# Kernel optimization log

Hardware: AMD Instinct MI355X
Metric: run time of the kernel (lower is better)

## Reference

```python
import jax, jax.numpy as jnp
import numpy as np

HID = 2048      # hidden_size
NH = 32         # num_heads
QLR = 1536      # q_lora_rank
KVLR = 512      # kv_lora_rank
DR = 64         # qk_rope_head_dim
DN = 128        # qk_nope_head_dim
DV = 128        # v_head_dim
DQK = DN + DR   # 192
EPS = 1e-6
ROPE_BASE = 10000.0


def rms_norm(x, w):
    return x * jax.lax.rsqrt(jnp.mean(x * x, axis=-1, keepdims=True) + EPS) * w


def apply_rope(x, pos):
    # x: [B, S, H, d] (non-interleaved / rotate-half convention), pos: [S]
    d = x.shape[-1]
    inv_freq = 1.0 / (ROPE_BASE ** (jnp.arange(0, d, 2, dtype=jnp.float32) / d))
    freqs = pos[:, None].astype(jnp.float32) * inv_freq      # [S, d/2]
    cos = jnp.cos(freqs)[None, :, None, :]                   # [1, S, 1, d/2]
    sin = jnp.sin(freqs)[None, :, None, :]
    x1, x2 = x[..., : d // 2], x[..., d // 2:]
    return jnp.concatenate([x1 * cos - x2 * sin, x1 * sin + x2 * cos], axis=-1)


def setup_inputs() -> dict:
    key = jax.random.key(0)
    ks = jax.random.split(key, 8)
    s = 0.02
    return {
        "hidden_states": jax.random.normal(ks[0], (1, 2048, HID), jnp.float32),
        "q_a_w":    jax.random.normal(ks[1], (HID, QLR), jnp.float32) * s,
        "q_a_ln_w": jnp.ones((QLR,), jnp.float32),
        "q_b_w":    jax.random.normal(ks[2], (QLR, NH * DQK), jnp.float32) * s,
        "kv_a_w":   jax.random.normal(ks[3], (HID, KVLR + DR), jnp.float32) * s,
        "kv_a_ln_w": jnp.ones((KVLR,), jnp.float32),
        "kv_b_w":   jax.random.normal(ks[4], (KVLR, NH * (DN + DV)), jnp.float32) * s,
        "o_w":      jax.random.normal(ks[5], (NH * DV, HID), jnp.float32) * s,
    }


def reference(hidden_states, q_a_w, q_a_ln_w, q_b_w, kv_a_w, kv_a_ln_w, kv_b_w, o_w):
    B, S, _ = hidden_states.shape
    # low-rank Q: down-proj -> RMSNorm -> up-proj
    q = rms_norm(hidden_states @ q_a_w, q_a_ln_w) @ q_b_w       # [B,S,NH*DQK]
    q = q.reshape(B, S, NH, DQK)
    q_pass, q_rot = q[..., :DN], q[..., DN:]
    # compressed KV + shared rope key
    ckv = hidden_states @ kv_a_w                                # [B,S,KVLR+DR]
    c_kv, k_rot = ckv[..., :KVLR], ckv[..., KVLR:]
    kv = rms_norm(c_kv, kv_a_ln_w) @ kv_b_w                     # [B,S,NH*(DN+DV)]
    kv = kv.reshape(B, S, NH, DN + DV)
    k_pass, v = kv[..., :DN], kv[..., DN:]
    # RoPE
    pos = jnp.arange(S)
    q_rot = apply_rope(q_rot, pos)                              # [B,S,NH,DR]
    k_rot = apply_rope(k_rot[:, :, None, :], pos)[:, :, 0, :]   # [B,S,DR] (shared head)
    # causal attention, scale = qk_head_dim**-0.5
    scale = DQK ** -0.5
    scores = (jnp.einsum('bqhd,bkhd->bhqk', q_pass, k_pass)
              + jnp.einsum('bqhd,bkd->bhqk', q_rot, k_rot)) * scale
    causal = jnp.tril(jnp.ones((S, S), dtype=bool))
    scores = jnp.where(causal[None, None], scores, jnp.finfo(scores.dtype).min)
    p = jax.nn.softmax(scores, axis=-1)
    out = jnp.einsum('bhqk,bkhd->bqhd', p, v).reshape(B, S, NH * DV)
    return out @ o_w
```

## Files before the change

### kernel.cpp

```cpp
#include <hip/hip_runtime.h>


typedef __bf16 bf16x8 __attribute__((ext_vector_type(8)));
typedef float  f32x4  __attribute__((ext_vector_type(4)));
typedef unsigned u32x4 __attribute__((ext_vector_type(4)));

#define GLOAD16(g, l)                                                          \
  __builtin_amdgcn_global_load_lds(                                            \
      (const __attribute__((address_space(1))) unsigned int*)(g),              \
      (__attribute__((address_space(3))) unsigned int*)(l), 16, 0, 0)

__device__ __forceinline__ unsigned short f2b(float f) {
  unsigned u = __builtin_bit_cast(unsigned, f);
  u += 0x7fffu + ((u >> 16) & 1u);
  return (unsigned short)(u >> 16);
}

__device__ __forceinline__ unsigned cvtpk(float lo, float hi) {
  unsigned r;
  asm("v_cvt_pk_bf16_f32 %0, %1, %2" : "=v"(r) : "v"(lo), "v"(hi));
  return r;
}

__device__ __forceinline__ void tc_body(const float* __restrict__ src,
// ... 31 lines not shown
    return;
  }
  b -= 4096;
  int tx = tid & 31, ty = tid >> 5;
  if (b < 3072)       { tc_body(qaw,  wcat,               2048, 1536, b & 63,  b >> 6, tx, ty); return; }
  b -= 3072;
  if (b < 1280)       { tc_body(kvaw, wcat + 1536UL*2048, 2048, 576,  b & 63,  b >> 6, tx, ty); return; }
  b -= 1280;
  if (b < 9216)       { tc_body(qbw,  qbT,                1536, 6144, b % 48,  b / 48, tx, ty); return; }
  b -= 9216;
  if (b < 4096)       { tc_body(kvbw, kvbT,               512,  8192, b & 15,  b >> 4, tx, ty); return; }
  b -= 4096;
  tc_body(ow, owT, 4096, 2048, b & 127, b >> 7, tx, ty);
}

__global__ __launch_bounds__(256) void rms2(const float* __restrict__ c0,
                                            const float* __restrict__ c1,
                                            const float* __restrict__ qw,
                                            const float* __restrict__ kvw,
                                            unsigned short* __restrict__ qan,
                                            unsigned short* __restrict__ ckvn,
                                            unsigned short* __restrict__ Kb) {
  int b = blockIdx.x, tid = threadIdx.x;
  __shared__ float red[4];
  if (b < 2048) {
    const float* x0 = c0 + (size_t)b * 2176;
    const float* x1 = c1 + (size_t)b * 2176;
    float vb[6], ss = 0.f;
#pragma unroll
    for (int j = 0; j < 6; j++) {
      float v = x0[tid + j * 256] + x1[tid + j * 256];
      vb[j] = v; ss += v * v;
    }
#pragma unroll
    for (int off = 1; off < 64; off <<= 1) ss += __shfl_xor(ss, off, 64);
    if ((tid & 63) == 0) red[tid >> 6] = ss;
    __syncthreads();
    ss = red[0] + red[1] + red[2] + red[3];
    float r = rsqrtf(ss / 1536.f + 1e-6f);
    unsigned short* orow = qan + (size_t)b * 1536;
#pragma unroll
    for (int j = 0; j < 6; j++)
      orow[tid + j * 256] = f2b(vb[j] * r * qw[tid + j * 256]);
  } else {
    int t = b - 2048;
    const float* x0 = c0 + (size_t)t * 2176 + 1536;
    const float* x1 = c1 + (size_t)t * 2176 + 1536;
    float vb[2], ss = 0.f;
#pragma unroll
    for (int j = 0; j < 2; j++) {
      float v = x0[tid + j * 256] + x1[tid + j * 256];
      vb[j] = v; ss += v * v;
    }
#pragma unroll
    for (int off = 1; off < 64; off <<= 1) ss += __shfl_xor(ss, off, 64);
    __shared__ unsigned short rot[64];
    if ((tid & 63) == 0) red[tid >> 6] = ss;
    __syncthreads();
    ss = red[0] + red[1] + red[2] + red[3];
    float r = rsqrtf(ss / 512.f + 1e-6f);
    unsigned short* orow = ckvn + (size_t)t * 512;
#pragma unroll
    for (int j = 0; j < 2; j++)
      orow[tid + j * 256] = f2b(vb[j] * r * kvw[tid + j * 256]);
    if (tid < 32) {
      float x1v = c0[(size_t)t * 2176 + 2048 + tid] + c1[(size_t)t * 2176 + 2048 + tid];
      float x2v = c0[(size_t)t * 2176 + 2080 + tid] + c1[(size_t)t * 2176 + 2080 + tid];
      float a = (float)t * exp2f(-(float)tid * 0.4152410118609203f);
      float cs = __cosf(a), sn = __sinf(a);
      rot[tid]      = f2b(x1v * cs - x2v * sn);
      rot[tid + 32] = f2b(x1v * sn + x2v * cs);
    }
    __syncthreads();
    for (int idx = tid; idx < 2048; idx += 256) {
      int h = idx >> 6, d = idx & 63;
      Kb[(size_t)t * 6144 + h * 192 + 128 + d] = rot[d];
    }
  }
}

__global__ __launch_bounds__(256) void addout(const float4* __restrict__ p,
                                              float4* __restrict__ o) {
  int i = blockIdx.x * 256 + threadIdx.x;
  float4 a = p[i], b = p[i + 1048576];
  float4 r; r.x = a.x + b.x; r.y = a.y + b.y; r.z = a.z + b.z; r.w = a.w + b.w;
  o[i] = r;
}

__global__ __launch_bounds__(256) void gemm_bt(const unsigned short* __restrict__ A,
                                               const unsigned short* __restrict__ Bt,
                                               float* __restrict__ Cp,
                                               int M, int N, int Ktot,
                                               int GX, int total) {
  __shared__ unsigned short As[4096];
  __shared__ unsigned short Bs[4096];
  const int tid = threadIdx.x;
  const int w = tid >> 6, lane = tid & 63;
  const int lr = lane & 15, lh = lane >> 4;
  const int lin = blockIdx.x, cpx = gridDim.x >> 3;
  int sid = (lin & 7) * cpx + (lin >> 3);
  const int s = (sid >= total);
  if (s) sid -= total;
  const int m0 = (sid / GX) * 128, n0 = (sid % GX) * 128;
  const int Kseg = Ktot >> 1;
  const unsigned short* Ab = A + (size_t)s * Kseg;
  const unsigned short* Bb = Bt + (size_t)s * Kseg;
  float* C = Cp + (size_t)s * M * N;
  const int wm = w >> 1, wn = w & 1;
  const int srow = lane >> 2;
  const int schunk = (lane & 3) ^ ((lane >> 3) & 3);
  const int swzr = (lr >> 1) & 3;

  f32x4 acc[4][4];
  const f32x4 z = {0.f, 0.f, 0.f, 0.f};
#pragma unroll
  for (int i = 0; i < 4; i++)
#pragma unroll
    for (int j = 0; j < 4; j++) acc[i][j] = z;

  for (int k0 = 0; k0 < Kseg; k0 += 32) {
#pragma unroll
    for (int c = 0; c < 2; c++) {
      GLOAD16(Ab + (size_t)(m0 + c * 64 + w * 16 + srow) * Ktot + k0 + schunk * 8,
              As + c * 2048 + w * 512);
      GLOAD16(Bb + (size_t)(n0 + c * 64 + w * 16 + srow) * Ktot + k0 + schunk * 8,
              Bs + c * 2048 + w * 512);
    }
    __syncthreads();
    bf16x8 a[4], b[4];
#pragma unroll
    for (int m = 0; m < 4; m++) {
      int row = wm * 64 + m * 16 + lr;
      a[m] = *(const bf16x8*)(As + row * 32 + ((lh ^ swzr) * 8));
    }
#pragma unroll
    for (int n = 0; n < 4; n++) {
      int row = wn * 64 + n * 16 + lr;
      b[n] = *(const bf16x8*)(Bs + row * 32 + ((lh ^ swzr) * 8));
    }
#pragma unroll
    for (int m = 0; m < 4; m++)
#pragma unroll
      for (int n = 0; n < 4; n++)
        acc[m][n] = __builtin_amdgcn_mfma_f32_16x16x32_bf16(a[m], b[n], acc[m][n], 0, 0, 0);
    __syncthreads();
  }
#pragma unroll
  for (int m = 0; m < 4; m++)
#pragma unroll
    for (int n = 0; n < 4; n++)
#pragma unroll
      for (int r = 0; r < 4; r++) {
        int row = m0 + wm * 64 + m * 16 + lh * 4 + r;
        int col = n0 + wn * 64 + n * 16 + lr;
        C[(size_t)row * N + col] = acc[m][n][r];
      }
}

__global__ __launch_bounds__(512) void gemm256m(
    const unsigned short* __restrict__ Aq, const unsigned short* __restrict__ Bq,
    unsigned short* __restrict__ Qb,
    const unsigned short* __restrict__ Akv, const unsigned short* __restrict__ Bkv,
    unsigned short* __restrict__ Kb, unsigned short* __restrict__ Vt) {
  __shared__ unsigned short lds[2][2][16384];
  const int tid = threadIdx.x;
  const int w = tid >> 6, lane = tid & 63;
  const int lr = lane & 15, lh = lane >> 4;
  const int wr = w >> 2, wc = w & 3;
  const int blk = blockIdx.x;
  const bool isq = blk < 192;
  const int bx = isq ? (blk % 24) : ((blk - 192) & 31);
  const int by = isq ? (blk / 24) : ((blk - 192) >> 5);
  const int K  = isq ? 1536 : 512;
  const int N  = isq ? 6144 : 8192;
  const unsigned short* A  = isq ? Aq : Akv;
  const unsigned short* Bt = isq ? Bq : Bkv;
  const int m0 = by * 256, n0 = bx * 256;

  int soff[2];
#pragma unroll
  for (int j = 0; j < 2; j++) {
    int c = j * 512 + tid;
    int row = c >> 3, p = c & 7;
    soff[j] = row * K + (p ^ (row & 7)) * 8;
  }
  const unsigned short* Abase = A + (size_t)m0 * K;
  const unsigned short* Bbase = Bt + (size_t)n0 * K;
  const int rswz = lr & 7;

#define STAGEOP(op, Base, kt, buf)                                             \
  {                                                                            \
    _Pragma("unroll") for (int hh = 0; hh < 2; hh++)                           \
    _Pragma("unroll") for (int j = 0; j < 2; j++)                              \
      GLOAD16(Base + (size_t)(hh * 128) * K + soff[j] + (kt) * 64,             \
              &lds[buf][op][(hh * 1024 + j * 512 + w * 64) * 8]);              \
  }
#define READA(mh, buf)                                                         \
  {                                                                            \
    _Pragma("unroll") for (int mi = 0; mi < 4; mi++)                           \
    _Pragma("unroll") for (int ks = 0; ks < 2; ks++)                           \
      af[mi][ks] = *(const bf16x8*)&lds[buf][0][                               \
          (wr * 128 + ((mh) * 4 + mi) * 16 + lr) * 64 +                        \
          (((ks * 4 + lh) ^ rswz) * 8)];                                       \
  }
#define READB(n, buf)                                                          \
  {                                                                            \
    _Pragma("unroll") for (int ks = 0; ks < 2; ks++)                           \
      bfr[n][ks] = *(const bf16x8*)&lds[buf][1][                               \
          (wc * 64 + (n) * 16 + lr) * 64 + (((ks * 4 + lh) ^ rswz) * 8)];      \
  }
#define MFMAQ(mh, nh)                                                          \
  {                                                                            \
    __builtin_amdgcn_s_setprio(1);                                             \
    _Pragma("unroll") for (int mi = 0; mi < 4; mi++)                           \
    _Pragma("unroll") for (int ni = 0; ni < 2; ni++)                           \
    _Pragma("unroll") for (int ks = 0; ks < 2; ks++)                           \
      acc[(mh) * 4 + mi][(nh) * 2 + ni] =                                      \
          __builtin_amdgcn_mfma_f32_16x16x32_bf16(                             \
              af[mi][ks], bfr[(nh) * 2 + ni][ks],                              \
              acc[(mh) * 4 + mi][(nh) * 2 + ni], 0, 0, 0);                     \
    __builtin_amdgcn_s_setprio(0);                                             \
  }

  f32x4 acc[8][4];
  const f32x4 z = {0.f, 0.f, 0.f, 0.f};
#pragma unroll
  for (int i = 0; i < 8; i++)
#pragma unroll
    for (int j = 0; j < 4; j++) acc[i][j] = z;

  STAGEOP(0, Abase, 0, 0);
  STAGEOP(1, Bbase, 0, 0);
  asm volatile("s_waitcnt vmcnt(0)" ::: "memory");
  __builtin_amdgcn_s_barrier();

  const int KT = K >> 6;
  for (int kt = 0; kt < KT; ++kt) {
    const int buf = kt & 1;
    const bool more = (kt + 1 < KT);
    bf16x8 af[4][2], bfr[4][2];
    READA(0, buf);
    READB(0, buf); READB(1, buf);
    if (more) STAGEOP(0, Abase, kt + 1, buf ^ 1);
    __builtin_amdgcn_s_barrier();
    MFMAQ(0, 0);
    __builtin_amdgcn_s_barrier();
    READB(2, buf); READB(3, buf);
    if (more) STAGEOP(1, Bbase, kt + 1, buf ^ 1);
    __builtin_amdgcn_s_barrier();
    MFMAQ(0, 1);
    __builtin_amdgcn_s_barrier();
    READA(1, buf);
    __builtin_amdgcn_s_barrier();
    MFMAQ(1, 1);
    __builtin_amdgcn_s_barrier();
    MFMAQ(1, 0);
    if (more) asm volatile("s_waitcnt vmcnt(0)" ::: "memory");
    __builtin_amdgcn_s_barrier();
  }
#undef STAGEOP
#undef READA
#undef READB
#undef MFMAQ

  if (isq) {
    const float kSc = 0.104126984f;
#pragma unroll
    for (int m = 0; m < 8; m++)
#pragma unroll
      for (int n = 0; n < 4; n++) {
        int colb = n0 + wc * 64 + n * 16;
        int sb = colb % 192;
        bool isrope = sb >= 128;
        bool first  = sb < 160;
        int col = colb + lr;
#pragma unroll
        for (int r = 0; r < 4; r++) {
          int row = m0 + wr * 128 + m * 16 + lh * 4 + r;
          float v = acc[m][n][r], o;
          if (!isrope) {
            o = v;
          } else {
            int ii = (col - 128) & 31;
            float ang = (float)row * exp2f(-(float)ii * 0.4152410118609203f);
            float cs = __cosf(ang), sn = __sinf(ang);
            float pa_ = acc[m][(n + 2) & 3][r];
            float pb_ = acc[m][(n + 6) & 3][r];
            float partner = first ? pa_ : pb_;
            o = first ? (v * cs - partner * sn) : (partner * sn + v * cs);
          }
          Qb[(size_t)row * 6144 + col] = f2b(o * kSc);
        }
      }
  } else {
    const int h = bx;
    unsigned short* Vlds = (unsigned short*)lds;
    if (wc < 2) {
#pragma unroll
      for (int m = 0; m < 8; m++)
#pragma unroll
        for (int n = 0; n < 4; n++) {
          int dd = wc * 64 + n * 16 + lr;
          int rowb = m0 + wr * 128 + m * 16 + lh * 4;
#pragma unroll
          for (int r = 0; r < 4; r++)
            Kb[(size_t)(rowb + r) * 6144 + h * 192 + dd] = f2b(acc[m][n][r]);
        }
    } else {
#pragma unroll
      for (int m = 0; m < 8; m++)
#pragma unroll
        for (int n = 0; n < 4; n++) {
          int dd = (wc - 2) * 64 + n * 16 + lr;
          int tl = wr * 128 + m * 16 + lh * 4;
          ushort4 pk;
          pk.x = f2b(acc[m][n][0]); pk.y = f2b(acc[m][n][1]);
          pk.z = f2b(acc[m][n][2]); pk.w = f2b(acc[m][n][3]);
          *(ushort4*)(Vlds + dd * 264 + tl) = pk;
        }
    }
    __syncthreads();
    {
      int r = tid >> 2, seg = tid & 3;
      const unsigned short* srcp = Vlds + r * 264 + seg * 64;
      unsigned short* dstp = Vt + (size_t)(h * 128 + r) * 2048 + m0 + seg * 64;
#pragma unroll
      for (int j = 0; j < 8; j++)
        *(int4*)(dstp + j * 8) = *(const int4*)(srcp + j * 8);
    }
  }
}

__global__ __launch_bounds__(512) void attn(const unsigned short* __restrict__ Qb,
                                            const unsigned short* __restrict__ Kb,
                                            const unsigned short* __restrict__ Vt,
                                            unsigned short* __restrict__ O) {
  __shared__ unsigned short Kl[2][12288];
  __shared__ unsigned short Vl[2][8192];
  const int tid = threadIdx.x;
  const int w = tid >> 6, lane = tid & 63;
  const int lr = lane & 15, lh = lane >> 4;
  const int b = blockIdx.x;
  const int x = b & 7, k = b >> 3;
  const int h = x + 8 * (k >> 4);
  const int ii = k & 15;
  int qi = (ii & 1) ? (15 - 2 * (ii >> 1)) : (2 * (ii >> 1));
  if (k & 32) qi = 15 - qi;
  const int q0 = qi * 128;
  const int qw = q0 + w * 16;
  const int qv = qw + lr;

  bf16x8 qf[6];
#pragma unroll
  for (int c = 0; c < 6; c++)
    qf[c] = *(const bf16x8*)(Qb + (size_t)(qw + lr) * 6144 + h * 192 + c * 32 + lh * 8);

  const unsigned short* Kbase = Kb + h * 192;
  const unsigned short* Vbase = Vt + (size_t)h * 128 * 2048;
  size_t ka[3];
#pragma unroll
  for (int j = 0; j < 3; j++) {
    int c = tid + j * 512;
    int r = c / 24, p = c - r * 24;
    ka[j] = (size_t)r * 6144 + (p ^ (r & 7)) * 8;
  }
  size_t va[2];
#pragma unroll
  for (int j = 0; j < 2; j++) {
    int c = tid + j * 512;
    int d = c >> 3, p = c & 7;
    va[j] = (size_t)d * 2048 + (p ^ (d & 7)) * 8;
  }

#define STAGE(T0, B)                                                           \
  {                                                                            \
    _Pragma("unroll") for (int j = 0; j < 3; j++)                              \
        GLOAD16(Kbase + (size_t)(T0) * 6144 + ka[j], &Kl[B][(tid + j * 512) * 8]); \
    _Pragma("unroll") for (int j = 0; j < 2; j++)                              \
        GLOAD16(Vbase + va[j] + (T0), &Vl[B][(tid + j * 512) * 8]);            \
  }

  f32x4 acc[8];
  const f32x4 z = {0.f, 0.f, 0.f, 0.f};
#pragma unroll
  for (int n = 0; n < 8; n++) acc[n] = z;
  float mrow = -1e30f, lrow = 0.f;
  const int swz = (lr & 7) * 8;
  const int cv0 = ((lh ^ (lr & 7)) * 8);
  const int cv1 = (((4 + lh) ^ (lr & 7)) * 8);
  const int sA = lr + 32 * (lh & 1), sB = sA + 16;

  const int nt = (q0 + 128) >> 6;
  STAGE(0, 0);
  __syncthreads();
  for (int it = 0; it < nt; ++it) {
    const int t0 = it << 6;
    const int cur = it & 1;
    if (it + 1 < nt) STAGE(t0 + 64, cur ^ 1);
    if (t0 <= qw + 15) {
      f32x4 s0 = z, s1 = z, s2 = z, s3 = z;
      __builtin_amdgcn_s_setprio(1);
#pragma unroll
      for (int c = 0; c < 6; c++) {
        int col = ((c * 4 + lh) * 8) ^ swz;
        bf16x8 k0 = *(const bf16x8*)(&Kl[cur][(lr)      * 192 + col]);
        bf16x8 k1 = *(const bf16x8*)(&Kl[cur][(16 + lr) * 192 + col]);
        bf16x8 k2 = *(const bf16x8*)(&Kl[cur][(32 + lr) * 192 + col]);
        bf16x8 k3 = *(const bf16x8*)(&Kl[cur][(48 + lr) * 192 + col]);
        s0 = __builtin_amdgcn_mfma_f32_16x16x32_bf16(k0, qf[c], s0, 0, 0, 0);
        s1 = __builtin_amdgcn_mfma_f32_16x16x32_bf16(k1, qf[c], s1, 0, 0, 0);
        s2 = __builtin_amdgcn_mfma_f32_16x16x32_bf16(k2, qf[c], s2, 0, 0, 0);
        s3 = __builtin_amdgcn_mfma_f32_16x16x32_bf16(k3, qf[c], s3, 0, 0, 0);
      }
      __builtin_amdgcn_s_setprio(0);
      const int tb = t0 + lh * 4;
      if (t0 + 63 > qw) {
#pragma unroll
        for (int r = 0; r < 4; r++) {
          s0[r] = (tb + r > qv)      ? -1e30f : s0[r];
          s1[r] = (tb + 16 + r > qv) ? -1e30f : s1[r];
          s2[r] = (tb + 32 + r > qv) ? -1e30f : s2[r];
          s3[r] = (tb + 48 + r > qv) ? -1e30f : s3[r];
        }
      }
      float mx = -1e30f;
#pragma unroll
      for (int r = 0; r < 4; r++)
        mx = fmaxf(mx, fmaxf(fmaxf(s0[r], s1[r]), fmaxf(s2[r], s3[r])));
      mx = fmaxf(mx, __shfl_xor(mx, 16, 64));
      mx = fmaxf(mx, __shfl_xor(mx, 32, 64));
      float ro = 1.f;
      bool resc = (mx - mrow) > 11.5f;
      if (resc) { ro = exp2f(mrow - mx); mrow = mx; }
      float p0[4], p1[4], p2[4], p3[4], ls = 0.f;
#pragma unroll
      for (int r = 0; r < 4; r++) {
        p0[r] = exp2f(s0[r] - mrow);
        p1[r] = exp2f(s1[r] - mrow);
        p2[r] = exp2f(s2[r] - mrow);
        p3[r] = exp2f(s3[r] - mrow);
        ls += (p0[r] + p1[r]) + (p2[r] + p3[r]);
      }
      lrow = lrow * ro + ls;
      if (__any(resc)) {
        float rs[4];
#pragma unroll
        for (int r = 0; r < 4; r++) rs[r] = __shfl(ro, lh * 4 + r, 16);
#pragma unroll
        for (int n = 0; n < 8; n++)
#pragma unroll
          for (int r = 0; r < 4; r++) acc[n][r] *= rs[r];
      }
      unsigned k0p = cvtpk(p0[0], p0[1]), k1p = cvtpk(p0[2], p0[3]);
      unsigned k2p = cvtpk(p1[0], p1[1]), k3p = cvtpk(p1[2], p1[3]);
      unsigned k4p = cvtpk(p2[0], p2[1]), k5p = cvtpk(p2[2], p2[3]);
      unsigned k6p = cvtpk(p3[0], p3[1]), k7p = cvtpk(p3[2], p3[3]);
      u32x4 w0, w1;
      {
        unsigned A0 = __shfl(k0p, sA, 64), A1 = __shfl(k1p, sA, 64);
        unsigned B0 = __shfl(k0p, sB, 64), B1 = __shfl(k1p, sB, 64);
        unsigned C0 = __shfl(k2p, sA, 64), C1 = __shfl(k3p, sA, 64);
        unsigned D0 = __shfl(k2p, sB, 64), D1 = __shfl(k3p, sB, 64);
        w0[0] = (lh < 2) ? A0 : C0;
        w0[1] = (lh < 2) ? A1 : C1;
        w0[2] = (lh < 2) ? B0 : D0;
        w0[3] = (lh < 2) ? B1 : D1;
      }
      {
        unsigned A0 = __shfl(k4p, sA, 64), A1 = __shfl(k5p, sA, 64);
        unsigned B0 = __shfl(k4p, sB, 64), B1 = __shfl(k5p, sB, 64);
        unsigned C0 = __shfl(k6p, sA, 64), C1 = __shfl(k7p, sA, 64);
        unsigned D0 = __shfl(k6p, sB, 64), D1 = __shfl(k7p, sB, 64);
        w1[0] = (lh < 2) ? A0 : C0;
        w1[1] = (lh < 2) ? A1 : C1;
        w1[2] = (lh < 2) ? B0 : D0;
        w1[3] = (lh < 2) ? B1 : D1;
      }
      bf16x8 pa0 = __builtin_bit_cast(bf16x8, w0);
      bf16x8 pa1 = __builtin_bit_cast(bf16x8, w1);
      __builtin_amdgcn_s_setprio(1);
#pragma unroll
      for (int n = 0; n < 8; n++) {
        bf16x8 vb0 = *(const bf16x8*)(&Vl[cur][(n * 16 + lr) * 64 + cv0]);
        bf16x8 vb1 = *(const bf16x8*)(&Vl[cur][(n * 16 + lr) * 64 + cv1]);
        acc[n] = __builtin_amdgcn_mfma_f32_16x16x32_bf16(pa0, vb0, acc[n], 0, 0, 0);
        acc[n] = __builtin_amdgcn_mfma_f32_16x16x32_bf16(pa1, vb1, acc[n], 0, 0, 0);
      }
      __builtin_amdgcn_s_setprio(0);
    }
    __syncthreads();
  }
#undef STAGE
  lrow += __shfl_xor(lrow, 16, 64);
  lrow += __shfl_xor(lrow, 32, 64);
  float invL = 1.f / lrow;
  float inv[4];
#pragma unroll
  for (int r = 0; r < 4; r++) inv[r] = __shfl(invL, lh * 4 + r, 16);
#pragma unroll
  for (int n = 0; n < 8; n++)
#pragma unroll
    for (int r = 0; r < 4; r++) {
      int q = qw + lh * 4 + r;
      O[(size_t)q * 4096 + h * 128 + n * 16 + lr] = f2b(acc[n][r] * inv[r]);
    }
}

extern "C" void kernel_launch(void* const* d_in, const int* in_sizes, int n_in,
                              void* d_out, int out_size, void* d_ws, size_t ws_size,
                              hipStream_t stream) {
  const float* hs      = (const float*)d_in[0];
  const float* q_a_w   = (const float*)d_in[1];
  const float* q_a_ln  = (const float*)d_in[2];
  const float* q_b_w   = (const float*)d_in[3];
  const float* kv_a_w  = (const float*)d_in[4];
  const float* kv_a_ln = (const float*)d_in[5];
  const float* kv_b_w  = (const float*)d_in[6];
  const float* o_w     = (const float*)d_in[7];
  float* out = (float*)d_out;

  char* ws = (char*)d_ws;
  size_t off = 0;
  auto alloc = [&](size_t bytes) {
    void* p = ws + off;
    off += (bytes + 255) & ~(size_t)255;
    return p;
  };
  unsigned short* wcat    = (unsigned short*)alloc(2176UL * 2048 * 2);
  unsigned short* q_b_wT  = (unsigned short*)alloc(6144UL * 1536 * 2);
  unsigned short* kv_b_wT = (unsigned short*)alloc(8192UL * 512 * 2);
  unsigned short* o_wT    = (unsigned short*)alloc(2048UL * 4096 * 2);
  unsigned short* hs_b    = (unsigned short*)alloc(2048UL * 2048 * 2);
  unsigned short* q_a_n   = (unsigned short*)alloc(2048UL * 1536 * 2);
  unsigned short* Qb      = (unsigned short*)alloc(2048UL * 6144 * 2);
  unsigned short* ckv_n   = (unsigned short*)alloc(2048UL * 512 * 2);
  unsigned short* Kb      = (unsigned short*)alloc(2048UL * 6144 * 2);
  unsigned short* Vt      = (unsigned short*)alloc(32UL * 128 * 2048 * 2);
  char* big = (char*)alloc(37748736UL + 2UL * 2048 * 2048 * 4);
  float*          Craw0    = (float*)big;
  float*          Craw1    = (float*)(big + 2048UL * 2176 * 4);
  unsigned short* attn_out = (unsigned short*)big;
  float*          OutP     = (float*)(big + 37748736UL);
  (void)ws_size; (void)in_sizes; (void)n_in; (void)out_size;

  dim3 b256(256), b512(512);
  prep<<<29952, b256, 0, stream>>>(hs, hs_b, q_a_w, kv_a_w, wcat,
                                   q_b_w, q_b_wT, kv_b_w, kv_b_wT, o_w, o_wT);
  gemm_bt<<<544, b256, 0, stream>>>(hs_b, wcat, Craw0, 2048, 2176, 2048, 17, 272);
  rms2<<<4096, b256, 0, stream>>>(Craw0, Craw1, q_a_ln, kv_a_ln, q_a_n, ckv_n, Kb);
  gemm256m<<<448, b512, 0, stream>>>(q_a_n, q_b_wT, Qb, ckv_n, kv_b_wT, Kb, Vt);
  attn<<<512, b512, 0, stream>>>(Qb, Kb, Vt, attn_out);
  gemm_bt<<<512, b256, 0, stream>>>(attn_out, o_wT, OutP, 2048, 2048, 4096, 16, 256);
  addout<<<4096, b256, 0, stream>>>((const float4*)OutP, (float4*)out);
}
```

Baseline: 298.2 us.

## Halve attention KV tile to 32 keys and split o-proj GEMM four ways

The attention kernel now stages 32-key K/V tiles instead of 64, halving LDS use and cutting the work per iteration to two score MFMAs and one PV MFMA per output block. The V LDS swizzle is redone for the narrower tile. This gives finer causal skipping and a lower LDS footprint per block, at the cost of twice as many loop iterations and barriers. Separately, the output projection GEMM becomes a 4-way split-K over 1024 blocks for more parallelism, writing its partials into the reused Qb buffer, with addout summing four partials instead of two.

```diff
diff --git a/kernel.cpp b/kernel.cpp
--- a/kernel.cpp
+++ b/kernel.cpp
@@ -137,8 +137,12 @@
 __global__ __launch_bounds__(256) void addout(const float4* __restrict__ p,
                                               float4* __restrict__ o) {
   int i = blockIdx.x * 256 + threadIdx.x;
-  float4 a = p[i], b = p[i + 1048576];
-  float4 r; r.x = a.x + b.x; r.y = a.y + b.y; r.z = a.z + b.z; r.w = a.w + b.w;
+  float4 a = p[i], b = p[i + 1048576], c = p[i + 2097152], d = p[i + 3145728];
+  float4 r;
+  r.x = (a.x + b.x) + (c.x + d.x);
+  r.y = (a.y + b.y) + (c.y + d.y);
+  r.z = (a.z + b.z) + (c.z + d.z);
+  r.w = (a.w + b.w) + (c.w + d.w);
   o[i] = r;
 }
 
@@ -146,7 +150,7 @@
                                                const unsigned short* __restrict__ Bt,
                                                float* __restrict__ Cp,
                                                int M, int N, int Ktot,
-                                               int GX, int total) {
+                                               int GX, int total, int splits) {
   __shared__ unsigned short As[4096];
   __shared__ unsigned short Bs[4096];
   const int tid = threadIdx.x;
@@ -154,10 +158,10 @@
   const int lr = lane & 15, lh = lane >> 4;
   const int lin = blockIdx.x, cpx = gridDim.x >> 3;
   int sid = (lin & 7) * cpx + (lin >> 3);
-  const int s = (sid >= total);
-  if (s) sid -= total;
+  const int s = sid / total;
+  sid -= s * total;
   const int m0 = (sid / GX) * 128, n0 = (sid % GX) * 128;
-  const int Kseg = Ktot >> 1;
+  const int Kseg = Ktot / splits;
   const unsigned short* Ab = A + (size_t)s * Kseg;
   const unsigned short* Bb = Bt + (size_t)s * Kseg;
   float* C = Cp + (size_t)s * M * N;
@@ -390,8 +394,8 @@
                                             const unsigned short* __restrict__ Kb,
                                             const unsigned short* __restrict__ Vt,
                                             unsigned short* __restrict__ O) {
-  __shared__ unsigned short Kl[2][12288];
-  __shared__ unsigned short Vl[2][8192];
+  __shared__ unsigned short Kl[2][6144];
+  __shared__ unsigned short Vl[2][4096];
   const int tid = threadIdx.x;
   const int w = tid >> 6, lane = tid & 63;
   const int lr = lane & 15, lh = lane >> 4;
@@ -412,27 +416,30 @@
 
   const unsigned short* Kbase = Kb + h * 192;
   const unsigned short* Vbase = Vt + (size_t)h * 128 * 2048;
-  size_t ka[3];
-#pragma unroll
-  for (int j = 0; j < 3; j++) {
-    int c = tid + j * 512;
+  size_t kga0, kga1 = 0;
+  {
+    int c = w * 64 + lane;
     int r = c / 24, p = c - r * 24;
-    ka[j] = (size_t)r * 6144 + (p ^ (r & 7)) * 8;
-  }
-  size_t va[2];
-#pragma unroll
-  for (int j = 0; j < 2; j++) {
-    int c = tid + j * 512;
-    int d = c >> 3, p = c & 7;
-    va[j] = (size_t)d * 2048 + (p ^ (d & 7)) * 8;
+    kga0 = (size_t)r * 6144 + (p ^ (r & 7)) * 8;
+  }
+  if (w < 4) {
+    int c = 512 + w * 64 + lane;
+    int r = c / 24, p = c - r * 24;
+    kga1 = (size_t)r * 6144 + (p ^ (r & 7)) * 8;
+  }
+  size_t vga;
+  {
+    int c = w * 64 + lane;
+    int d = c >> 2, p = c & 3;
+    vga = (size_t)d * 2048 + (p ^ ((d >> 1) & 3)) * 8;
   }
 
 #define STAGE(T0, B)                                                           \
   {                                                                            \
-    _Pragma("unroll") for (int j = 0; j < 3; j++)                              \
-        GLOAD16(Kbase + (size_t)(T0) * 6144 + ka[j], &Kl[B][(tid + j * 512) * 8]); \
-    _Pragma("unroll") for (int j = 0; j < 2; j++)                              \
-        GLOAD16(Vbase + va[j] + (T0), &Vl[B][(tid + j * 512) * 8]);            \
+    GLOAD16(Kbase + (size_t)(T0) * 6144 + kga0, &Kl[B][w * 512]);              \
+    if (w < 4)                                                                 \
+      GLOAD16(Kbase + (size_t)(T0) * 6144 + kga1, &Kl[B][4096 + w * 512]);     \
+    GLOAD16(Vbase + vga + (T0), &Vl[B][w * 512]);                              \
   }
 
   f32x4 acc[8];
@@ -441,60 +448,51 @@
   for (int n = 0; n < 8; n++) acc[n] = z;
   float mrow = -1e30f, lrow = 0.f;
   const int swz = (lr & 7) * 8;
-  const int cv0 = ((lh ^ (lr & 7)) * 8);
-  const int cv1 = (((4 + lh) ^ (lr & 7)) * 8);
+  const int vsw = (lh ^ ((lr >> 1) & 3)) * 8;
   const int sA = lr + 32 * (lh & 1), sB = sA + 16;
 
-  const int nt = (q0 + 128) >> 6;
+  const int nt = (q0 + 128) >> 5;
   STAGE(0, 0);
   __syncthreads();
   for (int it = 0; it < nt; ++it) {
-    const int t0 = it << 6;
+    const int t0 = it << 5;
     const int cur = it & 1;
-    if (it + 1 < nt) STAGE(t0 + 64, cur ^ 1);
+    if (it + 1 < nt) STAGE(t0 + 32, cur ^ 1);
     if (t0 <= qw + 15) {
-      f32x4 s0 = z, s1 = z, s2 = z, s3 = z;
+      f32x4 s0 = z, s1 = z;
       __builtin_amdgcn_s_setprio(1);
 #pragma unroll
       for (int c = 0; c < 6; c++) {
         int col = ((c * 4 + lh) * 8) ^ swz;
-        bf16x8 k0 = *(const bf16x8*)(&Kl[cur][(lr)      * 192 + col]);
+        bf16x8 k0 = *(const bf16x8*)(&Kl[cur][lr * 192 + col]);
         bf16x8 k1 = *(const bf16x8*)(&Kl[cur][(16 + lr) * 192 + col]);
-        bf16x8 k2 = *(const bf16x8*)(&Kl[cur][(32 + lr) * 192 + col]);
-        bf16x8 k3 = *(const bf16x8*)(&Kl[cur][(48 + lr) * 192 + col]);
         s0 = __builtin_amdgcn_mfma_f32_16x16x32_bf16(k0, qf[c], s0, 0, 0, 0);
         s1 = __builtin_amdgcn_mfma_f32_16x16x32_bf16(k1, qf[c], s1, 0, 0, 0);
-        s2 = __builtin_amdgcn_mfma_f32_16x16x32_bf16(k2, qf[c], s2, 0, 0, 0);
-        s3 = __builtin_amdgcn_mfma_f32_16x16x32_bf16(k3, qf[c], s3, 0, 0, 0);
       }
       __builtin_amdgcn_s_setprio(0);
       const int tb = t0 + lh * 4;
-      if (t0 + 63 > qw) {
+      if (t0 + 31 > qw) {
 #pragma unroll
         for (int r = 0; r < 4; r++) {
           s0[r] = (tb + r > qv)      ? -1e30f : s0[r];
           s1[r] = (tb + 16 + r > qv) ? -1e30f : s1[r];
-          s2[r] = (tb + 32 + r > qv) ? -1e30f : s2[r];
-          s3[r] = (tb + 48 + r > qv) ? -1e30f : s3[r];
         }
       }
       float mx = -1e30f;
 #pragma unroll
       for (int r = 0; r < 4; r++)
-        mx = fmaxf(mx, fmaxf(fmaxf(s0[r], s1[r]), fmaxf(s2[r], s3[r])));
+        mx = fmaxf(mx, fmaxf(s0[r], s1[r]));
       mx = fmaxf(mx, __shfl_xor(mx, 16, 64));
       mx = fmaxf(mx, __shfl_xor(mx, 32, 64));
       float ro = 1.f;
       bool resc = (mx - mrow) > 11.5f;
       if (resc) { ro = exp2f(mrow - mx); mrow = mx; }
-      float p0[4], p1[4], p2[4], p3[4], ls = 0.f;
+      float p0[4], p1[4], ls = 0.f;
 #pragma unroll
       for (int r = 0; r < 4; r++) {
         p0[r] = exp2f(s0[r] - mrow);
         p1[r] = exp2f(s1[r] - mrow);
-        p2[r] = exp2f(s2[r] - mrow);
-        p3[r] = exp2f(s3[r] - mrow);
-        ls += (p0[r] + p1[r]) + (p2[r] + p3[r]);
+        ls += p0[r] + p1[r];
       }
       lrow = lrow * ro + ls;
       if (__any(resc)) {
@@ -506,40 +504,23 @@
 #pragma unroll
           for (int r = 0; r < 4; r++) acc[n][r] *= rs[r];
       }
-      unsigned k0p = cvtpk(p0[0], p0[1]), k1p = cvtpk(p0[2], p0[3]);
-      unsigned k2p = cvtpk(p1[0], p1[1]), k3p = cvtpk(p1[2], p1[3]);
-      unsigned k4p = cvtpk(p2[0], p2[1]), k5p = cvtpk(p2[2], p2[3]);
-      unsigned k6p = cvtpk(p3[0], p3[1]), k7p = cvtpk(p3[2], p3[3]);
-      u32x4 w0, w1;
-      {
-        unsigned A0 = __shfl(k0p, sA, 64), A1 = __shfl(k1p, sA, 64);
-        unsigned B0 = __shfl(k0p, sB, 64), B1 = __shfl(k1p, sB, 64);
-        unsigned C0 = __shfl(k2p, sA, 64), C1 = __shfl(k3p, sA, 64);
-        unsigned D0 = __shfl(k2p, sB, 64), D1 = __shfl(k3p, sB, 64);
-        w0[0] = (lh < 2) ? A0 : C0;
-        w0[1] = (lh < 2) ? A1 : C1;
-        w0[2] = (lh < 2) ? B0 : D0;
-        w0[3] = (lh < 2) ? B1 : D1;
-      }
-      {
-        unsigned A0 = __shfl(k4p, sA, 64), A1 = __shfl(k5p, sA, 64);
-        unsigned B0 = __shfl(k4p, sB, 64), B1 = __shfl(k5p, sB, 64);
-        unsigned C0 = __shfl(k6p, sA, 64), C1 = __shfl(k7p, sA, 64);
-        unsigned D0 = __shfl(k6p, sB, 64), D1 = __shfl(k7p, sB, 64);
-        w1[0] = (lh < 2) ? A0 : C0;
-        w1[1] = (lh < 2) ? A1 : C1;
-        w1[2] = (lh < 2) ? B0 : D0;
-        w1[3] = (lh < 2) ? B1 : D1;
-      }
-      bf16x8 pa0 = __builtin_bit_cast(bf16x8, w0);
-      bf16x8 pa1 = __builtin_bit_cast(bf16x8, w1);
+      unsigned pk0 = cvtpk(p0[0], p0[1]), pk1 = cvtpk(p0[2], p0[3]);
+      unsigned pk2 = cvtpk(p1[0], p1[1]), pk3 = cvtpk(p1[2], p1[3]);
+      unsigned A0 = __shfl(pk0, sA, 64), A1 = __shfl(pk1, sA, 64);
+      unsigned B0 = __shfl(pk0, sB, 64), B1 = __shfl(pk1, sB, 64);
+      unsigned C0 = __shfl(pk2, sA, 64), C1 = __shfl(pk3, sA, 64);
+      unsigned D0 = __shfl(pk2, sB, 64), D1 = __shfl(pk3, sB, 64);
+      u32x4 pw;
+      pw[0] = (lh < 2) ? A0 : C0;
+      pw[1] = (lh < 2) ? A1 : C1;
+      pw[2] = (lh < 2) ? B0 : D0;
+      pw[3] = (lh < 2) ? B1 : D1;
+      bf16x8 pa = __builtin_bit_cast(bf16x8, pw);
       __builtin_amdgcn_s_setprio(1);
 #pragma unroll
       for (int n = 0; n < 8; n++) {
-        bf16x8 vb0 = *(const bf16x8*)(&Vl[cur][(n * 16 + lr) * 64 + cv0]);
-        bf16x8 vb1 = *(const bf16x8*)(&Vl[cur][(n * 16 + lr) * 64 + cv1]);
-        acc[n] = __builtin_amdgcn_mfma_f32_16x16x32_bf16(pa0, vb0, acc[n], 0, 0, 0);
-        acc[n] = __builtin_amdgcn_mfma_f32_16x16x32_bf16(pa1, vb1, acc[n], 0, 0, 0);
+        bf16x8 vb = *(const bf16x8*)(&Vl[cur][(n * 16 + lr) * 32 + vsw]);
+        acc[n] = __builtin_amdgcn_mfma_f32_16x16x32_bf16(pa, vb, acc[n], 0, 0, 0);
       }
       __builtin_amdgcn_s_setprio(0);
     }
@@ -591,20 +572,20 @@
   unsigned short* ckv_n   = (unsigned short*)alloc(2048UL * 512 * 2);
   unsigned short* Kb      = (unsigned short*)alloc(2048UL * 6144 * 2);
   unsigned short* Vt      = (unsigned short*)alloc(32UL * 128 * 2048 * 2);
-  char* big = (char*)alloc(37748736UL + 2UL * 2048 * 2048 * 4);
+  float*          OutP    = (float*)Qb;
+  char* big = (char*)alloc(2UL * 2048 * 2176 * 4);
   float*          Craw0    = (float*)big;
   float*          Craw1    = (float*)(big + 2048UL * 2176 * 4);
   unsigned short* attn_out = (unsigned short*)big;
-  float*          OutP     = (float*)(big + 37748736UL);
   (void)ws_size; (void)in_sizes; (void)n_in; (void)out_size;
 
   dim3 b256(256), b512(512);
   prep<<<29952, b256, 0, stream>>>(hs, hs_b, q_a_w, kv_a_w, wcat,
                                    q_b_w, q_b_wT, kv_b_w, kv_b_wT, o_w, o_wT);
-  gemm_bt<<<544, b256, 0, stream>>>(hs_b, wcat, Craw0, 2048, 2176, 2048, 17, 272);
+  gemm_bt<<<544, b256, 0, stream>>>(hs_b, wcat, Craw0, 2048, 2176, 2048, 17, 272, 2);
   rms2<<<4096, b256, 0, stream>>>(Craw0, Craw1, q_a_ln, kv_a_ln, q_a_n, ckv_n, Kb);
   gemm256m<<<448, b512, 0, stream>>>(q_a_n, q_b_wT, Qb, ckv_n, kv_b_wT, Kb, Vt);
   attn<<<512, b512, 0, stream>>>(Qb, Kb, Vt, attn_out);
-  gemm_bt<<<512, b256, 0, stream>>>(attn_out, o_wT, OutP, 2048, 2048, 4096, 16, 256);
+  gemm_bt<<<1024, b256, 0, stream>>>(attn_out, o_wT, OutP, 2048, 2048, 4096, 16, 256, 4);
   addout<<<4096, b256, 0, stream>>>((const float4*)OutP, (float4*)out);
 }
```

Result: slower. 322.3 us (+8.1%).

## Use 256x256-tile split-K=4 GEMM for output projection, reuse Qb as partial buffer

Applied to the files above, without the earlier changes.

Replaces the 128x128 split-K=2 output projection with a dedicated 256x256-tile kernel using 512 threads, double-buffered LDS and split-K of 4 across 256 blocks. The larger tiles raise arithmetic intensity per loaded byte. The reduction kernel now sums four partial planes instead of two. The fp32 partials go into the Qb buffer, which is no longer needed after attention, to shrink the workspace. The cost is twice the partial-sum traffic and fewer blocks per K slice.

```diff
diff --git a/kernel.cpp b/kernel.cpp
--- a/kernel.cpp
+++ b/kernel.cpp
@@ -137,8 +137,12 @@
 __global__ __launch_bounds__(256) void addout(const float4* __restrict__ p,
                                               float4* __restrict__ o) {
   int i = blockIdx.x * 256 + threadIdx.x;
-  float4 a = p[i], b = p[i + 1048576];
-  float4 r; r.x = a.x + b.x; r.y = a.y + b.y; r.z = a.z + b.z; r.w = a.w + b.w;
+  float4 a = p[i], b = p[i + 1048576], c = p[i + 2097152], d = p[i + 3145728];
+  float4 r;
+  r.x = (a.x + b.x) + (c.x + d.x);
+  r.y = (a.y + b.y) + (c.y + d.y);
+  r.z = (a.z + b.z) + (c.z + d.z);
+  r.w = (a.w + b.w) + (c.w + d.w);
   o[i] = r;
 }
 
@@ -146,7 +150,7 @@
                                                const unsigned short* __restrict__ Bt,
                                                float* __restrict__ Cp,
                                                int M, int N, int Ktot,
-                                               int GX, int total) {
+                                               int GX, int total, int splits) {
   __shared__ unsigned short As[4096];
   __shared__ unsigned short Bs[4096];
   const int tid = threadIdx.x;
@@ -154,10 +158,10 @@
   const int lr = lane & 15, lh = lane >> 4;
   const int lin = blockIdx.x, cpx = gridDim.x >> 3;
   int sid = (lin & 7) * cpx + (lin >> 3);
-  const int s = (sid >= total);
-  if (s) sid -= total;
+  const int s = sid / total;
+  sid -= s * total;
   const int m0 = (sid / GX) * 128, n0 = (sid % GX) * 128;
-  const int Kseg = Ktot >> 1;
+  const int Kseg = Ktot / splits;
   const unsigned short* Ab = A + (size_t)s * Kseg;
   const unsigned short* Bb = Bt + (size_t)s * Kseg;
   float* C = Cp + (size_t)s * M * N;
@@ -227,7 +231,6 @@
   const int bx = isq ? (blk % 24) : ((blk - 192) & 31);
   const int by = isq ? (blk / 24) : ((blk - 192) >> 5);
   const int K  = isq ? 1536 : 512;
-  const int N  = isq ? 6144 : 8192;
   const unsigned short* A  = isq ? Aq : Akv;
   const unsigned short* Bt = isq ? Bq : Bkv;
   const int m0 = by * 256, n0 = bx * 256;
@@ -384,6 +387,120 @@
         *(int4*)(dstp + j * 8) = *(const int4*)(srcp + j * 8);
     }
   }
+}
+
+__global__ __launch_bounds__(512) void gemm256_op(
+    const unsigned short* __restrict__ A, const unsigned short* __restrict__ Bt,
+    float* __restrict__ Cp) {
+  __shared__ unsigned short lds[2][2][16384];
+  const int tid = threadIdx.x;
+  const int w = tid >> 6, lane = tid & 63;
+  const int lr = lane & 15, lh = lane >> 4;
+  const int wr = w >> 2, wc = w & 3;
+  const int lin = blockIdx.x;
+  const int sid = (lin & 7) * 32 + (lin >> 3);
+  const int s = sid >> 6, rem = sid & 63;
+  const int m0 = (rem >> 3) * 256, n0 = (rem & 7) * 256;
+  const int Kst = 4096;
+  const int koff = s * 1024;
+
+  int soff[2];
+#pragma unroll
+  for (int j = 0; j < 2; j++) {
+    int c = j * 512 + tid;
+    int row = c >> 3, p = c & 7;
+    soff[j] = row * Kst + (p ^ (row & 7)) * 8;
+  }
+  const unsigned short* Abase = A + (size_t)m0 * Kst + koff;
+  const unsigned short* Bbase = Bt + (size_t)n0 * Kst + koff;
+  const int rswz = lr & 7;
+
+#define STAGEOP(op, Base, kt, buf)                                             \
+  {                                                                            \
+    _Pragma("unroll") for (int hh = 0; hh < 2; hh++)                           \
+    _Pragma("unroll") for (int j = 0; j < 2; j++)                              \
+      GLOAD16(Base + (size_t)(hh * 128) * Kst + soff[j] + (kt) * 64,           \
+              &lds[buf][op][(hh * 1024 + j * 512 + w * 64) * 8]);              \
+  }
+#define READA(mh, buf)                                                         \
+  {                                                                            \
+    _Pragma("unroll") for (int mi = 0; mi < 4; mi++)                           \
+    _Pragma("unroll") for (int ks = 0; ks < 2; ks++)                           \
+      af[mi][ks] = *(const bf16x8*)&lds[buf][0][                               \
+          (wr * 128 + ((mh) * 4 + mi) * 16 + lr) * 64 +                        \
+          (((ks * 4 + lh) ^ rswz) * 8)];                                       \
+  }
+#define READB(n, buf)                                                          \
+  {                                                                            \
+    _Pragma("unroll") for (int ks = 0; ks < 2; ks++)                           \
+      bfr[n][ks] = *(const bf16x8*)&lds[buf][1][                               \
+          (wc * 64 + (n) * 16 + lr) * 64 + (((ks * 4 + lh) ^ rswz) * 8)];      \
+  }
+#define MFMAQ(mh, nh)                                                          \
+  {                                                                            \
+    __builtin_amdgcn_s_setprio(1);                                             \
+    _Pragma("unroll") for (int mi = 0; mi < 4; mi++)                           \
+    _Pragma("unroll") for (int ni = 0; ni < 2; ni++)                           \
+    _Pragma("unroll") for (int ks = 0; ks < 2; ks++)                           \
+      acc[(mh) * 4 + mi][(nh) * 2 + ni] =                                      \
+          __builtin_amdgcn_mfma_f32_16x16x32_bf16(                             \
+              af[mi][ks], bfr[(nh) * 2 + ni][ks],                              \
+              acc[(mh) * 4 + mi][(nh) * 2 + ni], 0, 0, 0);                     \
+    __builtin_amdgcn_s_setprio(0);                                             \
+  }
+
+  f32x4 acc[8][4];
+  const f32x4 z = {0.f, 0.f, 0.f, 0.f};
+#pragma unroll
+  for (int i = 0; i < 8; i++)
+#pragma unroll
+    for (int j = 0; j < 4; j++) acc[i][j] = z;
+
+  STAGEOP(0, Abase, 0, 0);
+  STAGEOP(1, Bbase, 0, 0);
+  asm volatile("s_waitcnt vmcnt(0)" ::: "memory");
+  __builtin_amdgcn_s_barrier();
+
+  const int KT = 16;
+  for (int kt = 0; kt < KT; ++kt) {
+    const int buf = kt & 1;
+    const bool more = (kt + 1 < KT);
+    bf16x8 af[4][2], bfr[4][2];
+    READA(0, buf);
+    READB(0, buf); READB(1, buf);
+    if (more) STAGEOP(0, Abase, kt + 1, buf ^ 1);
+    __builtin_amdgcn_s_barrier();
+    MFMAQ(0, 0);
+    __builtin_amdgcn_s_barrier();
+    READB(2, buf); READB(3, buf);
+    if (more) STAGEOP(1, Bbase, kt + 1, buf ^ 1);
+    __builtin_amdgcn_s_barrier();
+    MFMAQ(0, 1);
+    __builtin_amdgcn_s_barrier();
+    READA(1, buf);
+    __builtin_amdgcn_s_barrier();
+    MFMAQ(1, 1);
+    __builtin_amdgcn_s_barrier();
+    MFMAQ(1, 0);
+    if (more) asm volatile("s_waitcnt vmcnt(0)" ::: "memory");
+    __builtin_amdgcn_s_barrier();
+  }
+#undef STAGEOP
+#undef READA
+#undef READB
+#undef MFMAQ
+
+  float* C = Cp + (size_t)s * 2048 * 2048;
+#pragma unroll
+  for (int m = 0; m < 8; m++)
+#pragma unroll
+    for (int n = 0; n < 4; n++)
+#pragma unroll
+      for (int r = 0; r < 4; r++) {
+        int row = m0 + wr * 128 + m * 16 + lh * 4 + r;
+        int col = n0 + wc * 64 + n * 16 + lr;
+        C[(size_t)row * 2048 + col] = acc[m][n][r];
+      }
 }
 
 __global__ __launch_bounds__(512) void attn(const unsigned short* __restrict__ Qb,
@@ -591,20 +708,20 @@
   unsigned short* ckv_n   = (unsigned short*)alloc(2048UL * 512 * 2);
   unsigned short* Kb      = (unsigned short*)alloc(2048UL * 6144 * 2);
   unsigned short* Vt      = (unsigned short*)alloc(32UL * 128 * 2048 * 2);
-  char* big = (char*)alloc(37748736UL + 2UL * 2048 * 2048 * 4);
+  float*          OutP    = (float*)Qb;
+  char* big = (char*)alloc(2UL * 2048 * 2176 * 4);
   float*          Craw0    = (float*)big;
   float*          Craw1    = (float*)(big + 2048UL * 2176 * 4);
   unsigned short* attn_out = (unsigned short*)big;
-  float*          OutP     = (float*)(big + 37748736UL);
   (void)ws_size; (void)in_sizes; (void)n_in; (void)out_size;
 
   dim3 b256(256), b512(512);
   prep<<<29952, b256, 0, stream>>>(hs, hs_b, q_a_w, kv_a_w, wcat,
                                    q_b_w, q_b_wT, kv_b_w, kv_b_wT, o_w, o_wT);
-  gemm_bt<<<544, b256, 0, stream>>>(hs_b, wcat, Craw0, 2048, 2176, 2048, 17, 272);
+  gemm_bt<<<544, b256, 0, stream>>>(hs_b, wcat, Craw0, 2048, 2176, 2048, 17, 272, 2);
   rms2<<<4096, b256, 0, stream>>>(Craw0, Craw1, q_a_ln, kv_a_ln, q_a_n, ckv_n, Kb);
   gemm256m<<<448, b512, 0, stream>>>(q_a_n, q_b_wT, Qb, ckv_n, kv_b_wT, Kb, Vt);
   attn<<<512, b512, 0, stream>>>(Qb, Kb, Vt, attn_out);
-  gemm_bt<<<512, b256, 0, stream>>>(attn_out, o_wT, OutP, 2048, 2048, 4096, 16, 256);
+  gemm256_op<<<256, b512, 0, stream>>>(attn_out, o_wT, OutP);
   addout<<<4096, b256, 0, stream>>>((const float4*)OutP, (float4*)out);
 }
```

Measured after the change: 287.2 us. -3.7%, faster.

## Use triple-buffered 256x256 GEMM core for up-proj and 4-way split-K output projection

Applied to the files above, without the earlier changes.

Replaces the two-stage, 64-wide-K pipeline in the up-projection GEMM with a shared 3-stage, 32-wide-K LDS ring that prefetches two tiles ahead and uses fewer barriers. The output projection moves from a 128x128 2-way split-K kernel to a 256x256 4-way split-K kernel built on the same core, and the reduction kernel now sums four partials. Partial outputs reuse the Q buffer's workspace to keep memory small. The aim is to hide global-load latency and raise MFMA density, at the cost of extra partial-sum traffic and a smaller K step per barrier.

```diff
diff --git a/kernel.cpp b/kernel.cpp
--- a/kernel.cpp
+++ b/kernel.cpp
@@ -137,8 +137,12 @@
 __global__ __launch_bounds__(256) void addout(const float4* __restrict__ p,
                                               float4* __restrict__ o) {
   int i = blockIdx.x * 256 + threadIdx.x;
-  float4 a = p[i], b = p[i + 1048576];
-  float4 r; r.x = a.x + b.x; r.y = a.y + b.y; r.z = a.z + b.z; r.w = a.w + b.w;
+  float4 a = p[i], b = p[i + 1048576], c = p[i + 2097152], d = p[i + 3145728];
+  float4 r;
+  r.x = (a.x + b.x) + (c.x + d.x);
+  r.y = (a.y + b.y) + (c.y + d.y);
+  r.z = (a.z + b.z) + (c.z + d.z);
+  r.w = (a.w + b.w) + (c.w + d.w);
   o[i] = r;
 }
 
@@ -146,7 +150,7 @@
                                                const unsigned short* __restrict__ Bt,
                                                float* __restrict__ Cp,
                                                int M, int N, int Ktot,
-                                               int GX, int total) {
+                                               int GX, int total, int splits) {
   __shared__ unsigned short As[4096];
   __shared__ unsigned short Bs[4096];
   const int tid = threadIdx.x;
@@ -154,10 +158,10 @@
   const int lr = lane & 15, lh = lane >> 4;
   const int lin = blockIdx.x, cpx = gridDim.x >> 3;
   int sid = (lin & 7) * cpx + (lin >> 3);
-  const int s = (sid >= total);
-  if (s) sid -= total;
+  const int s = sid / total;
+  sid -= s * total;
   const int m0 = (sid / GX) * 128, n0 = (sid % GX) * 128;
-  const int Kseg = Ktot >> 1;
+  const int Kseg = Ktot / splits;
   const unsigned short* Ab = A + (size_t)s * Kseg;
   const unsigned short* Bb = Bt + (size_t)s * Kseg;
   float* C = Cp + (size_t)s * M * N;
@@ -212,12 +216,53 @@
       }
 }
 
+#define G256_CORE(Abase, Bbase, Kst, KT)                                       \
+  int soff[2];                                                                 \
+  _Pragma("unroll") for (int j = 0; j < 2; j++) {                              \
+    int c = j * 512 + tid;                                                     \
+    int row = c >> 2, p = c & 3;                                               \
+    soff[j] = row * (Kst) + (p ^ ((row >> 1) & 3)) * 8;                        \
+  }                                                                            \
+  const int rk = ((lr >> 1) & 3);                                              \
+  f32x4 acc[8][4];                                                             \
+  {                                                                            \
+    const f32x4 zz = {0.f, 0.f, 0.f, 0.f};                                     \
+    _Pragma("unroll") for (int i = 0; i < 8; i++)                              \
+    _Pragma("unroll") for (int j = 0; j < 4; j++) acc[i][j] = zz;              \
+  }                                                                            \
+  STAGE32(0, 0);                                                               \
+  STAGE32(1, 1);                                                               \
+  asm volatile("s_waitcnt vmcnt(4)" ::: "memory");                             \
+  __builtin_amdgcn_s_barrier();                                                \
+  int cur = 0, nxt = 2;                                                        \
+  for (int kt = 0; kt < (KT); ++kt) {                                          \
+    if (kt + 2 < (KT)) STAGE32(kt + 2, nxt);                                   \
+    bf16x8 af[8], bfr[4];                                                      \
+    _Pragma("unroll") for (int f = 0; f < 8; f++)                              \
+      af[f] = *(const bf16x8*)&lds[cur][0][                                    \
+          (wr * 128 + f * 16 + lr) * 32 + ((lh ^ rk) * 8)];                    \
+    _Pragma("unroll") for (int n = 0; n < 4; n++)                              \
+      bfr[n] = *(const bf16x8*)&lds[cur][1][                                   \
+          (wc * 64 + n * 16 + lr) * 32 + ((lh ^ rk) * 8)];                     \
+    __builtin_amdgcn_s_setprio(1);                                             \
+    _Pragma("unroll") for (int f = 0; f < 8; f++)                              \
+    _Pragma("unroll") for (int n = 0; n < 4; n++)                              \
+      acc[f][n] = __builtin_amdgcn_mfma_f32_16x16x32_bf16(                     \
+          af[f], bfr[n], acc[f][n], 0, 0, 0);                                  \
+    __builtin_amdgcn_s_setprio(0);                                             \
+    if (kt + 2 < (KT)) asm volatile("s_waitcnt vmcnt(4)" ::: "memory");        \
+    else               asm volatile("s_waitcnt vmcnt(0)" ::: "memory");        \
+    __builtin_amdgcn_s_barrier();                                              \
+    cur = (cur == 2) ? 0 : cur + 1;                                            \
+    nxt = (nxt == 2) ? 0 : nxt + 1;                                            \
+  }
+
 __global__ __launch_bounds__(512) void gemm256m(
     const unsigned short* __restrict__ Aq, const unsigned short* __restrict__ Bq,
     unsigned short* __restrict__ Qb,
     const unsigned short* __restrict__ Akv, const unsigned short* __restrict__ Bkv,
     unsigned short* __restrict__ Kb, unsigned short* __restrict__ Vt) {
-  __shared__ unsigned short lds[2][2][16384];
+  __shared__ unsigned short lds[3][2][8192];
   const int tid = threadIdx.x;
   const int w = tid >> 6, lane = tid & 63;
   const int lr = lane & 15, lh = lane >> 4;
@@ -227,96 +272,23 @@
   const int bx = isq ? (blk % 24) : ((blk - 192) & 31);
   const int by = isq ? (blk / 24) : ((blk - 192) >> 5);
   const int K  = isq ? 1536 : 512;
-  const int N  = isq ? 6144 : 8192;
   const unsigned short* A  = isq ? Aq : Akv;
   const unsigned short* Bt = isq ? Bq : Bkv;
   const int m0 = by * 256, n0 = bx * 256;
-
-  int soff[2];
-#pragma unroll
-  for (int j = 0; j < 2; j++) {
-    int c = j * 512 + tid;
-    int row = c >> 3, p = c & 7;
-    soff[j] = row * K + (p ^ (row & 7)) * 8;
-  }
   const unsigned short* Abase = A + (size_t)m0 * K;
   const unsigned short* Bbase = Bt + (size_t)n0 * K;
-  const int rswz = lr & 7;
-
-#define STAGEOP(op, Base, kt, buf)                                             \
+
+#define STAGE32(kt, buf)                                                       \
   {                                                                            \
-    _Pragma("unroll") for (int hh = 0; hh < 2; hh++)                           \
-    _Pragma("unroll") for (int j = 0; j < 2; j++)                              \
-      GLOAD16(Base + (size_t)(hh * 128) * K + soff[j] + (kt) * 64,             \
-              &lds[buf][op][(hh * 1024 + j * 512 + w * 64) * 8]);              \
-  }
-#define READA(mh, buf)                                                         \
-  {                                                                            \
-    _Pragma("unroll") for (int mi = 0; mi < 4; mi++)                           \
-    _Pragma("unroll") for (int ks = 0; ks < 2; ks++)                           \
-      af[mi][ks] = *(const bf16x8*)&lds[buf][0][                               \
-          (wr * 128 + ((mh) * 4 + mi) * 16 + lr) * 64 +                        \
-          (((ks * 4 + lh) ^ rswz) * 8)];                                       \
-  }
-#define READB(n, buf)                                                          \
-  {                                                                            \
-    _Pragma("unroll") for (int ks = 0; ks < 2; ks++)                           \
-      bfr[n][ks] = *(const bf16x8*)&lds[buf][1][                               \
-          (wc * 64 + (n) * 16 + lr) * 64 + (((ks * 4 + lh) ^ rswz) * 8)];      \
-  }
-#define MFMAQ(mh, nh)                                                          \
-  {                                                                            \
-    __builtin_amdgcn_s_setprio(1);                                             \
-    _Pragma("unroll") for (int mi = 0; mi < 4; mi++)                           \
-    _Pragma("unroll") for (int ni = 0; ni < 2; ni++)                           \
-    _Pragma("unroll") for (int ks = 0; ks < 2; ks++)                           \
-      acc[(mh) * 4 + mi][(nh) * 2 + ni] =                                      \
-          __builtin_amdgcn_mfma_f32_16x16x32_bf16(                             \
-              af[mi][ks], bfr[(nh) * 2 + ni][ks],                              \
-              acc[(mh) * 4 + mi][(nh) * 2 + ni], 0, 0, 0);                     \
-    __builtin_amdgcn_s_setprio(0);                                             \
-  }
-
-  f32x4 acc[8][4];
-  const f32x4 z = {0.f, 0.f, 0.f, 0.f};
-#pragma unroll
-  for (int i = 0; i < 8; i++)
-#pragma unroll
-    for (int j = 0; j < 4; j++) acc[i][j] = z;
-
-  STAGEOP(0, Abase, 0, 0);
-  STAGEOP(1, Bbase, 0, 0);
-  asm volatile("s_waitcnt vmcnt(0)" ::: "memory");
-  __builtin_amdgcn_s_barrier();
-
-  const int KT = K >> 6;
-  for (int kt = 0; kt < KT; ++kt) {
-    const int buf = kt & 1;
-    const bool more = (kt + 1 < KT);
-    bf16x8 af[4][2], bfr[4][2];
-    READA(0, buf);
-    READB(0, buf); READB(1, buf);
-    if (more) STAGEOP(0, Abase, kt + 1, buf ^ 1);
-    __builtin_amdgcn_s_barrier();
-    MFMAQ(0, 0);
-    __builtin_amdgcn_s_barrier();
-    READB(2, buf); READB(3, buf);
-    if (more) STAGEOP(1, Bbase, kt + 1, buf ^ 1);
-    __builtin_amdgcn_s_barrier();
-    MFMAQ(0, 1);
-    __builtin_amdgcn_s_barrier();
-    READA(1, buf);
-    __builtin_amdgcn_s_barrier();
-    MFMAQ(1, 1);
-    __builtin_amdgcn_s_barrier();
-    MFMAQ(1, 0);
-    if (more) asm volatile("s_waitcnt vmcnt(0)" ::: "memory");
-    __builtin_amdgcn_s_barrier();
-  }
-#undef STAGEOP
-#undef READA
-#undef READB
-#undef MFMAQ
+    _Pragma("unroll") for (int j = 0; j < 2; j++) {                            \
+      GLOAD16(Abase + soff[j] + (kt) * 32, &lds[buf][0][(j * 512 + tid) * 8]); \
+      GLOAD16(Bbase + soff[j] + (kt) * 32, &lds[buf][1][(j * 512 + tid) * 8]); \
+    }                                                                          \
+  }
+
+  const int KT = K >> 5;
+  G256_CORE(Abase, Bbase, K, KT)
+#undef STAGE32
 
   if (isq) {
     const float kSc = 0.104126984f;
@@ -384,6 +356,47 @@
         *(int4*)(dstp + j * 8) = *(const int4*)(srcp + j * 8);
     }
   }
+}
+
+__global__ __launch_bounds__(512) void gemm256_op(
+    const unsigned short* __restrict__ A, const unsigned short* __restrict__ Bt,
+    float* __restrict__ Cp) {
+  __shared__ unsigned short lds[3][2][8192];
+  const int tid = threadIdx.x;
+  const int w = tid >> 6, lane = tid & 63;
+  const int lr = lane & 15, lh = lane >> 4;
+  const int wr = w >> 2, wc = w & 3;
+  const int lin = blockIdx.x;
+  const int sid = (lin & 7) * 32 + (lin >> 3);
+  const int s = sid >> 6, rem = sid & 63;
+  const int m0 = (rem >> 3) * 256, n0 = (rem & 7) * 256;
+  const int Kst = 4096;
+  const int koff = s * 1024;
+  const unsigned short* Abase = A + (size_t)m0 * Kst + koff;
+  const unsigned short* Bbase = Bt + (size_t)n0 * Kst + koff;
+
+#define STAGE32(kt, buf)                                                       \
+  {                                                                            \
+    _Pragma("unroll") for (int j = 0; j < 2; j++) {                            \
+      GLOAD16(Abase + soff[j] + (kt) * 32, &lds[buf][0][(j * 512 + tid) * 8]); \
+      GLOAD16(Bbase + soff[j] + (kt) * 32, &lds[buf][1][(j * 512 + tid) * 8]); \
+    }                                                                          \
+  }
+
+  G256_CORE(Abase, Bbase, Kst, 32)
+#undef STAGE32
+
+  float* C = Cp + (size_t)s * 2048 * 2048;
+#pragma unroll
+  for (int m = 0; m < 8; m++)
+#pragma unroll
+    for (int n = 0; n < 4; n++)
+#pragma unroll
+      for (int r = 0; r < 4; r++) {
+        int row = m0 + wr * 128 + m * 16 + lh * 4 + r;
+        int col = n0 + wc * 64 + n * 16 + lr;
+        C[(size_t)row * 2048 + col] = acc[m][n][r];
+      }
 }
 
 __global__ __launch_bounds__(512) void attn(const unsigned short* __restrict__ Qb,
@@ -591,20 +604,20 @@
   unsigned short* ckv_n   = (unsigned short*)alloc(2048UL * 512 * 2);
   unsigned short* Kb      = (unsigned short*)alloc(2048UL * 6144 * 2);
   unsigned short* Vt      = (unsigned short*)alloc(32UL * 128 * 2048 * 2);
-  char* big = (char*)alloc(37748736UL + 2UL * 2048 * 2048 * 4);
+  float*          OutP    = (float*)Qb;
+  char* big = (char*)alloc(2UL * 2048 * 2176 * 4);
   float*          Craw0    = (float*)big;
   float*          Craw1    = (float*)(big + 2048UL * 2176 * 4);
   unsigned short* attn_out = (unsigned short*)big;
-  float*          OutP     = (float*)(big + 37748736UL);
   (void)ws_size; (void)in_sizes; (void)n_in; (void)out_size;
 
   dim3 b256(256), b512(512);
   prep<<<29952, b256, 0, stream>>>(hs, hs_b, q_a_w, kv_a_w, wcat,
                                    q_b_w, q_b_wT, kv_b_w, kv_b_wT, o_w, o_wT);
-  gemm_bt<<<544, b256, 0, stream>>>(hs_b, wcat, Craw0, 2048, 2176, 2048, 17, 272);
+  gemm_bt<<<544, b256, 0, stream>>>(hs_b, wcat, Craw0, 2048, 2176, 2048, 17, 272, 2);
   rms2<<<4096, b256, 0, stream>>>(Craw0, Craw1, q_a_ln, kv_a_ln, q_a_n, ckv_n, Kb);
   gemm256m<<<448, b512, 0, stream>>>(q_a_n, q_b_wT, Qb, ckv_n, kv_b_wT, Kb, Vt);
   attn<<<512, b512, 0, stream>>>(Qb, Kb, Vt, attn_out);
-  gemm_bt<<<512, b256, 0, stream>>>(attn_out, o_wT, OutP, 2048, 2048, 4096, 16, 256);
+  gemm256_op<<<256, b512, 0, stream>>>(attn_out, o_wT, OutP);
   addout<<<4096, b256, 0, stream>>>((const float4*)OutP, (float4*)out);
 }
```

Result: no change. 293.6 us (-1.5%).
